# Kernel optimization log

Measured on AMD Instinct MI355X. Metric: run time of the kernel, lower is better.

The kernel has to match this reference:

```python
import jax, jax.numpy as jnp
import numpy as np

NA = 50000
NB = 50000
E = 800000
D = 256


def setup_inputs() -> dict:
    key = jax.random.key(0)
    ks = jax.random.split(key, 7)
    feature_a = jax.random.normal(ks[0], (NA, D), dtype=jnp.float32)
    feature_b = jax.random.normal(ks[1], (NB, D), dtype=jnp.float32)
    # Linear(b_dim, b_dim): store weight pre-transposed so new_emb = feature_b @ W + b
    W = jax.random.normal(ks[2], (D, D), dtype=jnp.float32) * (1.0 / np.sqrt(D))
    b = jnp.zeros((D,), dtype=jnp.float32)
    # kaiming-normal-ish init for attention vector a: [a_dim + b_dim, 1]
    a = jax.random.normal(ks[3], (2 * D, 1), dtype=jnp.float32) * np.sqrt(2.0 / (2 * D))
    edge_src = jnp.sort(jax.random.randint(ks[4], (E,), 0, NA, dtype=jnp.int32)).astype(jnp.int64)
    edge_dst = jax.random.randint(ks[5], (E,), 0, NB, dtype=jnp.int64)
    return {
        "feature_a": feature_a,
        "feature_b": feature_b,
        "W": W,
        "b": b,
        "a": a,
        "edge_src": edge_src,
        "edge_dst": edge_dst,
        "node_num_a": NA,
        "node_num_b": NB,
    }


def reference(feature_a, feature_b, W, b, a, edge_src, edge_dst, node_num_a, node_num_b):
    # new_emb = out_mlp_layer(feature_b)
    new_emb = feature_b @ W + b  # [Nb, D]

    # cat([feature_a[src], new_emb[dst]]) @ a  ==  (feature_a @ a_top)[src] + (new_emb @ a_bot)[dst]
    a_dim = feature_a.shape[1]
    a_top = a[:a_dim, 0]   # [a_dim]
    a_bot = a[a_dim:, 0]   # [b_dim]
    s_a = feature_a @ a_top   # [Na]
    s_b = new_emb @ a_bot     # [Nb]
    logits = s_a[edge_src] + s_b[edge_dst]  # [E]

    # exp(elu(x, alpha=0.1))
    elu = jnp.where(logits > 0, logits, 0.1 * jnp.expm1(logits))
    score = jnp.exp(elu)  # [E]

    # sparse mm: weighted aggregation of new_emb over edges, grouped by src
    msg = score[:, None] * new_emb[edge_dst]  # [E, D]
    agg = jax.ops.segment_sum(msg, edge_src, num_segments=node_num_a)       # [Na, D]
    row_sum = jax.ops.segment_sum(score, edge_src, num_segments=node_num_a)  # [Na]
    row_sum = jnp.where(row_sum == 0, 1.0, row_sum)[:, None]
    return agg / row_sum
```

## Files before the change

kernel.cpp:

```cpp
#include <hip/hip_runtime.h>
#include <cstdint>

#define NA_N 50000
#define NB_N 50000
#define NE_N 800000
#define DD 256

using bf8   = __attribute__((ext_vector_type(8))) short;
using f32x4 = __attribute__((ext_vector_type(4))) float;
using u16x8 = __attribute__((ext_vector_type(8))) ushort;

__device__ __forceinline__ ushort f2bf(float f) {
    uint u = __float_as_uint(f);
    uint r = (u + 0x7fffu + ((u >> 16) & 1u)) >> 16;
    return (ushort)r;
}
__device__ __forceinline__ float bf2f(ushort u) {
    return __uint_as_float(((uint)u) << 16);
}

__global__ __launch_bounds__(256) void prep_k(const float* __restrict__ W,
    ushort* __restrict__ Wt, const int* __restrict__ esrc,
    int* __restrict__ row_start)
{
    if (blockIdx.x < 16) {
        __shared__ float T[64][65];
        const int bi = blockIdx.x & 3;
        const int bj = blockIdx.x >> 2;
        const int lane = threadIdx.x & 63, w = threadIdx.x >> 6;
        for (int i = w; i < 64; i += 4)
            T[i][lane] = W[(size_t)(bi * 64 + i) * DD + bj * 64 + lane];
        __syncthreads();
        for (int i = w; i < 64; i += 4)
            Wt[(size_t)(bj * 64 + i) * DD + bi * 64 + lane] = f2bf(T[lane][i]);
    } else {
        int e = (blockIdx.x - 16) * 256 + threadIdx.x;
        if (e >= NE_N) return;
        int s    = esrc[e];
        int prev = (e == 0) ? -1 : esrc[e - 1];
        for (int r = prev + 1; r <= s; r++) row_start[r] = e;
        if (e == NE_N - 1)
            for (int r = s + 1; r <= NA_N; r++) row_start[r] = NE_N;
    }
}

__global__ __launch_bounds__(256) void gemm_mfma(
    const float* __restrict__ A, const ushort* __restrict__ Wt,
    const float* __restrict__ bias, const float* __restrict__ a_bot,
    ushort* __restrict__ C, float* __restrict__ s_b)
{
    __shared__ ushort As[64 * 264];
    __shared__ float  sdot[4][64];
    const int t  = threadIdx.x;
    const int r0 = blockIdx.x * 64;

#pragma unroll
    for (int i = 0; i < 16; i++) {
        int flat = i * 256 + t;
        int row  = flat >> 6;
        int c4   = flat & 63;
        int gr   = r0 + row; if (gr >= NB_N) gr = 0;
        float4 v = ((const float4*)(A + (size_t)gr * DD))[c4];
        ushort4 b;
        b.x = f2bf(v.x); b.y = f2bf(v.y); b.z = f2bf(v.z); b.w = f2bf(v.w);
        *(ushort4*)&As[row * 264 + c4 * 4] = b;
    }
    __syncthreads();

    const int lane = t & 63;
    const int wv   = t >> 6;
    const int lr   = lane & 15;
    const int lk   = (lane >> 4) * 8;

    f32x4 acc[4][4];
#pragma unroll
    for (int m = 0; m < 4; m++)
#pragma unroll
        for (int n = 0; n < 4; n++) acc[m][n] = (f32x4){0.f, 0.f, 0.f, 0.f};

#pragma unroll
    for (int ks = 0; ks < 8; ks++) {
        const int k0 = ks * 32;
        bf8 af[4], bb[4];
#pragma unroll
        for (int m = 0; m < 4; m++)
            af[m] = *(const bf8*)&As[(m * 16 + lr) * 264 + k0 + lk];
#pragma unroll
        for (int n = 0; n < 4; n++) {
            int col = wv * 64 + n * 16 + lr;
            bb[n] = *(const bf8*)&Wt[(size_t)col * DD + k0 + lk];
        }
#pragma unroll
        for (int m = 0; m < 4; m++)
#pragma unroll
            for (int n = 0; n < 4; n++)
                acc[m][n] = __builtin_amdgcn_mfma_f32_16x16x32_bf16(
                    af[m], bb[n], acc[m][n], 0, 0, 0);
    }

    float abv[4];
#pragma unroll
    for (int n = 0; n < 4; n++) abv[n] = a_bot[wv * 64 + n * 16 + lr];

    float part[4][4];
#pragma unroll
    for (int m = 0; m < 4; m++)
#pragma unroll
        for (int r = 0; r < 4; r++) part[m][r] = 0.f;

#pragma unroll
    for (int m = 0; m < 4; m++)
#pragma unroll
        for (int n = 0; n < 4; n++) {
            int   col = wv * 64 + n * 16 + lr;
            float bv  = bias[col];
#pragma unroll
            for (int r = 0; r < 4; r++) {
                int   rowg = r0 + m * 16 + (lane >> 4) * 4 + r;
                float v    = acc[m][n][r] + bv;
                if (rowg < NB_N) C[(size_t)rowg * DD + col] = f2bf(v);
                part[m][r] = fmaf(v, abv[n], part[m][r]);
            }
        }

#pragma unroll
    for (int m = 0; m < 4; m++)
#pragma unroll
        for (int r = 0; r < 4; r++) {
#pragma unroll
            for (int off = 1; off < 16; off <<= 1)
                part[m][r] += __shfl_xor(part[m][r], off, 64);
        }
    if (lr == 0) {
#pragma unroll
        for (int m = 0; m < 4; m++)
#pragma unroll
            for (int r = 0; r < 4; r++)
                sdot[wv][m * 16 + (lane >> 4) * 4 + r] = part[m][r];
    }
    __syncthreads();
    if (t < 64) {
        int rowg = r0 + t;
        if (rowg < NB_N)
            s_b[rowg] = sdot[0][t] + sdot[1][t] + sdot[2][t] + sdot[3][t];
    }
}

__global__ __launch_bounds__(256) void edge_agg6(
    const int* __restrict__ edst, const int* __restrict__ row_start,
    const float* __restrict__ fa, const float* __restrict__ a_top,
    const float* __restrict__ sb, const ushort* __restrict__ emb,
    float* __restrict__ out)
{
    const int lane = threadIdx.x & 63;
    const int a    = blockIdx.x * 4 + (threadIdx.x >> 6);
    if (a >= NA_N) return;

    float4 av = ((const float4*)(fa + (size_t)a * DD))[lane];
    float4 tv = ((const float4*)a_top)[lane];
    float  sa_a = av.x * tv.x + av.y * tv.y + av.z * tv.z + av.w * tv.w;
#pragma unroll
    for (int off = 1; off < 64; off <<= 1) sa_a += __shfl_xor(sa_a, off, 64);

    const int g = lane >> 4;
    const int c = lane & 15;
    const int beg = row_start[a], end = row_start[a + 1];

    float accA[8], accB[8];
#pragma unroll
    for (int j = 0; j < 8; j++) { accA[j] = 0.f; accB[j] = 0.f; }
    float rs = 0.f;

    if (beg < end) {
        const int last = end - 1;

        int   pc  = beg + g;
        int   pn  = pc + 4;
        int   dc  = edst[min(pc, last)];
        int   dn  = edst[min(pn, last)];
        float sbc = sb[dc];
        float sbn = sb[dn];
        const ushort* rc = emb + (size_t)dc * DD + c * 16;
        u16x8 ua = *(const u16x8*)rc;
        u16x8 ub = *(const u16x8*)(rc + 8);

#pragma unroll 2
        for (int e = beg; e < end; e += 4) {
            const ushort* rn = emb + (size_t)dn * DD + c * 16;
            u16x8 na = *(const u16x8*)rn;
            u16x8 nb = *(const u16x8*)(rn + 8);
            int   p2  = pn + 4;
            int   d2  = edst[min(p2, last)];
            float sb2 = sb[d2];

            float lg = sa_a + sbc;
            float el = lg > 0.f ? lg : 0.1f * (__expf(lg) - 1.f);
            float s  = (pc < end) ? __expf(el) : 0.f;

#pragma unroll
            for (int j = 0; j < 8; j++) {
                accA[j] = fmaf(s, bf2f(ua[j]), accA[j]);
                accB[j] = fmaf(s, bf2f(ub[j]), accB[j]);
            }
            rs += s;

            pc = pn;  dc = dn;  sbc = sbn;
            ua = na;  ub = nb;
            pn = p2;  dn = d2;  sbn = sb2;
        }
    }

#pragma unroll
    for (int j = 0; j < 8; j++) {
        accA[j] += __shfl_xor(accA[j], 16, 64);
        accA[j] += __shfl_xor(accA[j], 32, 64);
        accB[j] += __shfl_xor(accB[j], 16, 64);
        accB[j] += __shfl_xor(accB[j], 32, 64);
    }
    rs += __shfl_xor(rs, 16, 64);
    rs += __shfl_xor(rs, 32, 64);

    if (g == 0) {
        const float inv = (rs == 0.f) ? 1.f : (1.f / rs);
        float* op = out + (size_t)a * DD + c * 16;
        float4 o0 = { accA[0] * inv, accA[1] * inv, accA[2] * inv, accA[3] * inv };
        float4 o1 = { accA[4] * inv, accA[5] * inv, accA[6] * inv, accA[7] * inv };
        float4 o2 = { accB[0] * inv, accB[1] * inv, accB[2] * inv, accB[3] * inv };
        float4 o3 = { accB[4] * inv, accB[5] * inv, accB[6] * inv, accB[7] * inv };
        *(float4*)(op + 0)  = o0;
        *(float4*)(op + 4)  = o1;
        *(float4*)(op + 8)  = o2;
        *(float4*)(op + 12) = o3;
    }
}

extern "C" void kernel_launch(void* const* d_in, const int* in_sizes, int n_in,
                              void* d_out, int out_size, void* d_ws, size_t ws_size,
                              hipStream_t stream)
{
    const float* fa   = (const float*)d_in[0];
    const float* fb   = (const float*)d_in[1];
    const float* W    = (const float*)d_in[2];
    const float* bias = (const float*)d_in[3];
    const float* avec = (const float*)d_in[4];
    const int*   esrc = (const int*)d_in[5];
    const int*   edst = (const int*)d_in[6];
    float*       out  = (float*)d_out;

    char*   ws        = (char*)d_ws;
    ushort* emb_b     = (ushort*)ws;
    float*  s_b       = (float*)(ws + (size_t)NB_N * DD * 2);
    int*    row_start = (int*)(s_b + NB_N);
    ushort* Wt        = (ushort*)(row_start + NA_N + 2);

    prep_k   <<<16 + (NE_N + 255) / 256, 256, 0, stream>>>(W, Wt, esrc, row_start);
    gemm_mfma<<<(NB_N + 63) / 64, 256, 0, stream>>>(fb, Wt, bias, avec + DD,
                                                    emb_b, s_b);
    edge_agg6<<<(NA_N + 3) / 4, 256, 0, stream>>>(edst, row_start, fa, avec,
                                                  s_b, emb_b, out);
}
```

Baseline: 108.5 us.

## Recast edge aggregation as MFMA with one-hot score matrix and async LDS staging

Replaces the per-row wave aggregation with a block that handles 16 source rows at once. Each chunk of 32 edges forms a sparse 16x32 score matrix (bf16 one-hot by source), and the gathered destination embeddings are multiplied by it with MFMA. The embeddings are staged into double-buffered LDS through global_load_lds and read back with transposed ds_read, and the row sums come from an extra MFMA against a ones vector. This trades scalar FMAs for matrix ops and overlaps gathers with compute, but it rounds scores to bf16 and adds block-wide barriers per chunk.

```diff
diff --git a/kernel.cpp b/kernel.cpp
--- a/kernel.cpp
+++ b/kernel.cpp
@@ -8,15 +8,12 @@
 
 using bf8   = __attribute__((ext_vector_type(8))) short;
 using f32x4 = __attribute__((ext_vector_type(4))) float;
-using u16x8 = __attribute__((ext_vector_type(8))) ushort;
+using u32x2 = __attribute__((ext_vector_type(2))) unsigned int;
 
 __device__ __forceinline__ ushort f2bf(float f) {
     uint u = __float_as_uint(f);
     uint r = (u + 0x7fffu + ((u >> 16) & 1u)) >> 16;
     return (ushort)r;
-}
-__device__ __forceinline__ float bf2f(ushort u) {
-    return __uint_as_float(((uint)u) << 16);
 }
 
 __global__ __launch_bounds__(256) void prep_k(const float* __restrict__ W,
@@ -146,92 +143,155 @@
     }
 }
 
-__global__ __launch_bounds__(256) void edge_agg6(
-    const int* __restrict__ edst, const int* __restrict__ row_start,
+__global__ __launch_bounds__(256) void edge_mfma(
+    const int* __restrict__ esrc, const int* __restrict__ edst,
+    const int* __restrict__ row_start,
     const float* __restrict__ fa, const float* __restrict__ a_top,
     const float* __restrict__ sb, const ushort* __restrict__ emb,
     float* __restrict__ out)
 {
-    const int lane = threadIdx.x & 63;
-    const int a    = blockIdx.x * 4 + (threadIdx.x >> 6);
-    if (a >= NA_N) return;
-
-    float4 av = ((const float4*)(fa + (size_t)a * DD))[lane];
-    float4 tv = ((const float4*)a_top)[lane];
-    float  sa_a = av.x * tv.x + av.y * tv.y + av.z * tv.z + av.w * tv.w;
-#pragma unroll
-    for (int off = 1; off < 64; off <<= 1) sa_a += __shfl_xor(sa_a, off, 64);
-
-    const int g = lane >> 4;
-    const int c = lane & 15;
-    const int beg = row_start[a], end = row_start[a + 1];
-
-    float accA[8], accB[8];
-#pragma unroll
-    for (int j = 0; j < 8; j++) { accA[j] = 0.f; accB[j] = 0.f; }
-    float rs = 0.f;
-
-    if (beg < end) {
-        const int last = end - 1;
-
-        int   pc  = beg + g;
-        int   pn  = pc + 4;
-        int   dc  = edst[min(pc, last)];
-        int   dn  = edst[min(pn, last)];
-        float sbc = sb[dc];
-        float sbn = sb[dn];
-        const ushort* rc = emb + (size_t)dc * DD + c * 16;
-        u16x8 ua = *(const u16x8*)rc;
-        u16x8 ub = *(const u16x8*)(rc + 8);
-
-#pragma unroll 2
-        for (int e = beg; e < end; e += 4) {
-            const ushort* rn = emb + (size_t)dn * DD + c * 16;
-            u16x8 na = *(const u16x8*)rn;
-            u16x8 nb = *(const u16x8*)(rn + 8);
-            int   p2  = pn + 4;
-            int   d2  = edst[min(p2, last)];
-            float sb2 = sb[d2];
-
-            float lg = sa_a + sbc;
-            float el = lg > 0.f ? lg : 0.1f * (__expf(lg) - 1.f);
-            float s  = (pc < end) ? __expf(el) : 0.f;
-
+    __shared__ ushort Bt[2][8192];
+    __shared__ float  sa_sh[16];
+    const int t = threadIdx.x, lane = t & 63, wv = t >> 6;
+    const int a0 = blockIdx.x * 16;
+
+    {
+        int r  = t >> 4;
+        int cs = (t & 15) * 16;
+        const float4* fr = (const float4*)(fa + (size_t)(a0 + r) * DD + cs);
+        const float4* tv = (const float4*)(a_top + cs);
+        float p = 0.f;
+#pragma unroll
+        for (int j = 0; j < 4; j++) {
+            float4 x = fr[j], y = tv[j];
+            p += x.x * y.x + x.y * y.y + x.z * y.z + x.w * y.w;
+        }
+        p += __shfl_xor(p, 1, 64); p += __shfl_xor(p, 2, 64);
+        p += __shfl_xor(p, 4, 64); p += __shfl_xor(p, 8, 64);
+        if ((t & 15) == 0) sa_sh[r] = p;
+    }
+    __syncthreads();
+    const float sa_lane = sa_sh[lane & 15];
+
+    const int beg  = row_start[a0], end = row_start[a0 + 16];
+    const int nch  = (end - beg + 31) >> 5;
+    const int el   = lane & 31;
+    const int last = end - 1;
+
+    f32x4 acc0 = {0,0,0,0}, acc1 = {0,0,0,0}, acc2 = {0,0,0,0},
+          acc3 = {0,0,0,0}, racc = {0,0,0,0};
+
+    const uint b0  = (uint)(uintptr_t)&Bt[0][0];
+    const uint trb = b0 + (uint)((lane >> 4) * 4096 + wv * 512 + (lane & 15) * 8);
+
+    bf8 onesb;
+    {
+        short o = (lane & 15) == 0 ? (short)0x3F80 : (short)0;
+#pragma unroll
+        for (int j = 0; j < 8; j++) onesb[j] = o;
+    }
+
+#define STAGE(BQ, DREG)                                                        \
+    {                                                                          \
+        _Pragma("unroll")                                                      \
+        for (int i_ = 0; i_ < 4; i_++) {                                       \
+            int W_  = wv * 4 + i_;                                             \
+            int k_  = ((W_ >> 1) << 2) | ((lane >> 1) & 3);                    \
+            int dk_ = __shfl((DREG), k_, 64);                                  \
+            const ushort* gs_ = emb + (size_t)dk_ * DD                         \
+                + (W_ & 1) * 128 + ((lane >> 3) & 7) * 16 + (lane & 1) * 8;    \
+            __builtin_amdgcn_global_load_lds(                                  \
+                (const __attribute__((address_space(1))) void*)(uintptr_t)gs_, \
+                (__attribute__((address_space(3))) void*)(uint)((BQ) + (uint)(W_ * 1024)), \
+                16, 0, 0);                                                     \
+        }                                                                      \
+    }
+
+    if (nch > 0) {
+        int   i0   = min(beg + el, last);
+        int   sr_c = esrc[i0] - a0;
+        int   d0   = edst[i0];
+        int   i1   = min(beg + 32 + el, last);
+        int   d_n  = edst[i1];
+        int   sr_n = esrc[i1] - a0;
+        float sb_c = sb[d0];
+        STAGE(b0, d0);
+
+        for (int tc = 0; tc < nch; ++tc) {
+            const int p = tc & 1;
+
+            bool  val = (beg + tc * 32 + el) < end;
+            float lg  = __shfl(sa_lane, sr_c, 64) + sb_c;
+            float elu = lg > 0.f ? lg : 0.1f * (__expf(lg) - 1.f);
+            float s   = val ? __expf(elu) : 0.f;
+            uint pack = (uint)f2bf(s) | ((uint)sr_c << 16);
+            bf8 af;
 #pragma unroll
             for (int j = 0; j < 8; j++) {
-                accA[j] = fmaf(s, bf2f(ua[j]), accA[j]);
-                accB[j] = fmaf(s, bf2f(ub[j]), accB[j]);
+                uint v = (uint)__shfl((int)pack, ((lane >> 4) << 3) + j, 64);
+                af[j]  = (short)(((v >> 16) == (uint)(lane & 15))
+                                     ? (ushort)(v & 0xFFFFu) : (ushort)0);
             }
-            rs += s;
-
-            pc = pn;  dc = dn;  sbc = sbn;
-            ua = na;  ub = nb;
-            pn = p2;  dn = d2;  sbn = sb2;
-        }
-    }
-
-#pragma unroll
-    for (int j = 0; j < 8; j++) {
-        accA[j] += __shfl_xor(accA[j], 16, 64);
-        accA[j] += __shfl_xor(accA[j], 32, 64);
-        accB[j] += __shfl_xor(accB[j], 16, 64);
-        accB[j] += __shfl_xor(accB[j], 32, 64);
-    }
-    rs += __shfl_xor(rs, 16, 64);
-    rs += __shfl_xor(rs, 32, 64);
-
-    if (g == 0) {
-        const float inv = (rs == 0.f) ? 1.f : (1.f / rs);
-        float* op = out + (size_t)a * DD + c * 16;
-        float4 o0 = { accA[0] * inv, accA[1] * inv, accA[2] * inv, accA[3] * inv };
-        float4 o1 = { accA[4] * inv, accA[5] * inv, accA[6] * inv, accA[7] * inv };
-        float4 o2 = { accB[0] * inv, accB[1] * inv, accB[2] * inv, accB[3] * inv };
-        float4 o3 = { accB[4] * inv, accB[5] * inv, accB[6] * inv, accB[7] * inv };
-        *(float4*)(op + 0)  = o0;
-        *(float4*)(op + 4)  = o1;
-        *(float4*)(op + 8)  = o2;
-        *(float4*)(op + 12) = o3;
-    }
+
+            const bool more = (tc + 1) < nch;
+            int d_nn = 0, sr_nn = 0; float sb_nn = 0.f;
+            if (more) {
+                sb_nn   = sb[d_n];
+                int i2  = min(beg + (tc + 2) * 32 + el, last);
+                d_nn    = edst[i2];
+                sr_nn   = esrc[i2] - a0;
+                uint bq = b0 + (uint)((p ^ 1) * 16384);
+                STAGE(bq, d_n);
+                asm volatile("s_waitcnt vmcnt(7)" ::: "memory");
+            } else {
+                asm volatile("s_waitcnt vmcnt(0)" ::: "memory");
+            }
+            __builtin_amdgcn_s_barrier();
+
+            const uint base = trb + (uint)(p * 16384);
+            u32x2 t0, t1, t2, t3, t4, t5, t6, t7;
+            asm volatile("ds_read_b64_tr_b16 %0, %1" : "=v"(t0) : "v"(base));
+            asm volatile("ds_read_b64_tr_b16 %0, %1" : "=v"(t1) : "v"(base + 2048u));
+            asm volatile("ds_read_b64_tr_b16 %0, %1" : "=v"(t2) : "v"(base + 128u));
+            asm volatile("ds_read_b64_tr_b16 %0, %1" : "=v"(t3) : "v"(base + 2176u));
+            asm volatile("ds_read_b64_tr_b16 %0, %1" : "=v"(t4) : "v"(base + 256u));
+            asm volatile("ds_read_b64_tr_b16 %0, %1" : "=v"(t5) : "v"(base + 2304u));
+            asm volatile("ds_read_b64_tr_b16 %0, %1" : "=v"(t6) : "v"(base + 384u));
+            asm volatile("ds_read_b64_tr_b16 %0, %1" : "=v"(t7) : "v"(base + 2432u));
+            asm volatile("s_waitcnt lgkmcnt(0)" ::: "memory");
+            __builtin_amdgcn_sched_barrier(0);
+
+            union { bf8 v; u32x2 h[2]; } U;
+            bf8 bf0, bf1, bf2, bf3;
+            U.h[0] = t0; U.h[1] = t1; bf0 = U.v;
+            U.h[0] = t2; U.h[1] = t3; bf1 = U.v;
+            U.h[0] = t4; U.h[1] = t5; bf2 = U.v;
+            U.h[0] = t6; U.h[1] = t7; bf3 = U.v;
+
+            acc0 = __builtin_amdgcn_mfma_f32_16x16x32_bf16(af, bf0, acc0, 0, 0, 0);
+            acc1 = __builtin_amdgcn_mfma_f32_16x16x32_bf16(af, bf1, acc1, 0, 0, 0);
+            acc2 = __builtin_amdgcn_mfma_f32_16x16x32_bf16(af, bf2, acc2, 0, 0, 0);
+            acc3 = __builtin_amdgcn_mfma_f32_16x16x32_bf16(af, bf3, acc3, 0, 0, 0);
+            racc = __builtin_amdgcn_mfma_f32_16x16x32_bf16(af, onesb, racc, 0, 0, 0);
+
+            __builtin_amdgcn_s_barrier();
+
+            sr_c = sr_n; sb_c = sb_nn; d_n = d_nn; sr_n = sr_nn;
+        }
+    }
+
+#pragma unroll
+    for (int reg = 0; reg < 4; reg++) {
+        float rsv = __shfl(racc[reg], lane & 48, 64);
+        float iv  = (rsv == 0.f) ? 0.f : (1.f / rsv);
+        int   row = a0 + (lane >> 4) * 4 + reg;
+        float* op = out + (size_t)row * DD + wv * 64 + (lane & 15);
+        op[0]  = acc0[reg] * iv;
+        op[16] = acc1[reg] * iv;
+        op[32] = acc2[reg] * iv;
+        op[48] = acc3[reg] * iv;
+    }
+#undef STAGE
 }
 
 extern "C" void kernel_launch(void* const* d_in, const int* in_sizes, int n_in,
@@ -256,6 +316,6 @@
     prep_k   <<<16 + (NE_N + 255) / 256, 256, 0, stream>>>(W, Wt, esrc, row_start);
     gemm_mfma<<<(NB_N + 63) / 64, 256, 0, stream>>>(fb, Wt, bias, avec + DD,
                                                     emb_b, s_b);
-    edge_agg6<<<(NA_N + 3) / 4, 256, 0, stream>>>(edst, row_start, fa, avec,
-                                                  s_b, emb_b, out);
-}
+    edge_mfma<<<NA_N / 16, 256, 0, stream>>>(esrc, edst, row_start, fa, avec,
+                                             s_b, emb_b, out);
+}
```

New measurement: 113.6 us. 1.05x slower.

## Move row_start build into GEMM launch and use nontemporal loads/stores

Applied to the files above, without the earlier changes.

Moves the CSR row_start construction out of the W-transpose prep kernel into extra blocks of the GEMM launch, so the prep kernel is tiny and the edge scan runs alongside the GEMM. It also marks streaming reads of feature_b, feature_a and edge_dst, and the output writes, as nontemporal to reduce cache pollution. The GEMM kernel now carries extra blocks with an early-exit path, which could change scheduling. Nontemporal hints may help or hurt the cache behaviour of the gather-heavy aggregation kernel.

```diff
diff --git a/kernel.cpp b/kernel.cpp
--- a/kernel.cpp
+++ b/kernel.cpp
@@ -5,6 +5,7 @@
 #define NB_N 50000
 #define NE_N 800000
 #define DD 256
+#define GEMM_NBLK 782
 
 using bf8   = __attribute__((ext_vector_type(8))) short;
 using f32x4 = __attribute__((ext_vector_type(4))) float;
@@ -20,37 +21,39 @@
 }
 
 __global__ __launch_bounds__(256) void prep_k(const float* __restrict__ W,
-    ushort* __restrict__ Wt, const int* __restrict__ esrc,
-    int* __restrict__ row_start)
-{
-    if (blockIdx.x < 16) {
-        __shared__ float T[64][65];
-        const int bi = blockIdx.x & 3;
-        const int bj = blockIdx.x >> 2;
-        const int lane = threadIdx.x & 63, w = threadIdx.x >> 6;
-        for (int i = w; i < 64; i += 4)
-            T[i][lane] = W[(size_t)(bi * 64 + i) * DD + bj * 64 + lane];
-        __syncthreads();
-        for (int i = w; i < 64; i += 4)
-            Wt[(size_t)(bj * 64 + i) * DD + bi * 64 + lane] = f2bf(T[lane][i]);
-    } else {
-        int e = (blockIdx.x - 16) * 256 + threadIdx.x;
+                                              ushort* __restrict__ Wt)
+{
+    __shared__ float T[64][65];
+    const int bi = blockIdx.x & 3;
+    const int bj = blockIdx.x >> 2;
+    const int lane = threadIdx.x & 63, w = threadIdx.x >> 6;
+    for (int i = w; i < 64; i += 4)
+        T[i][lane] = W[(size_t)(bi * 64 + i) * DD + bj * 64 + lane];
+    __syncthreads();
+    for (int i = w; i < 64; i += 4)
+        Wt[(size_t)(bj * 64 + i) * DD + bi * 64 + lane] = f2bf(T[lane][i]);
+}
+
+__global__ __launch_bounds__(256) void gemm_mfma(
+    const float* __restrict__ A, const ushort* __restrict__ Wt,
+    const float* __restrict__ bias, const float* __restrict__ a_bot,
+    ushort* __restrict__ C, float* __restrict__ s_b,
+    const int* __restrict__ esrc, int* __restrict__ row_start)
+{
+    __shared__ ushort As[64 * 264];
+    __shared__ float  sdot[4][64];
+
+    if (blockIdx.x >= GEMM_NBLK) {
+        int e = (blockIdx.x - GEMM_NBLK) * 256 + threadIdx.x;
         if (e >= NE_N) return;
         int s    = esrc[e];
         int prev = (e == 0) ? -1 : esrc[e - 1];
         for (int r = prev + 1; r <= s; r++) row_start[r] = e;
         if (e == NE_N - 1)
             for (int r = s + 1; r <= NA_N; r++) row_start[r] = NE_N;
-    }
-}
-
-__global__ __launch_bounds__(256) void gemm_mfma(
-    const float* __restrict__ A, const ushort* __restrict__ Wt,
-    const float* __restrict__ bias, const float* __restrict__ a_bot,
-    ushort* __restrict__ C, float* __restrict__ s_b)
-{
-    __shared__ ushort As[64 * 264];
-    __shared__ float  sdot[4][64];
+        return;
+    }
+
     const int t  = threadIdx.x;
     const int r0 = blockIdx.x * 64;
 
@@ -60,9 +63,10 @@
         int row  = flat >> 6;
         int c4   = flat & 63;
         int gr   = r0 + row; if (gr >= NB_N) gr = 0;
-        float4 v = ((const float4*)(A + (size_t)gr * DD))[c4];
+        f32x4 v = __builtin_nontemporal_load(
+                      ((const f32x4*)(A + (size_t)gr * DD)) + c4);
         ushort4 b;
-        b.x = f2bf(v.x); b.y = f2bf(v.y); b.z = f2bf(v.z); b.w = f2bf(v.w);
+        b.x = f2bf(v[0]); b.y = f2bf(v[1]); b.z = f2bf(v[2]); b.w = f2bf(v[3]);
         *(ushort4*)&As[row * 264 + c4 * 4] = b;
     }
     __syncthreads();
@@ -146,7 +150,7 @@
     }
 }
 
-__global__ __launch_bounds__(256) void edge_agg6(
+__global__ __launch_bounds__(256) void edge_agg7(
     const int* __restrict__ edst, const int* __restrict__ row_start,
     const float* __restrict__ fa, const float* __restrict__ a_top,
     const float* __restrict__ sb, const ushort* __restrict__ emb,
@@ -156,9 +160,9 @@
     const int a    = blockIdx.x * 4 + (threadIdx.x >> 6);
     if (a >= NA_N) return;
 
-    float4 av = ((const float4*)(fa + (size_t)a * DD))[lane];
-    float4 tv = ((const float4*)a_top)[lane];
-    float  sa_a = av.x * tv.x + av.y * tv.y + av.z * tv.z + av.w * tv.w;
+    f32x4 av = __builtin_nontemporal_load(((const f32x4*)(fa + (size_t)a * DD)) + lane);
+    f32x4 tv = *(((const f32x4*)a_top) + lane);
+    float sa_a = av[0] * tv[0] + av[1] * tv[1] + av[2] * tv[2] + av[3] * tv[3];
 #pragma unroll
     for (int off = 1; off < 64; off <<= 1) sa_a += __shfl_xor(sa_a, off, 64);
 
@@ -176,8 +180,8 @@
 
         int   pc  = beg + g;
         int   pn  = pc + 4;
-        int   dc  = edst[min(pc, last)];
-        int   dn  = edst[min(pn, last)];
+        int   dc  = __builtin_nontemporal_load(edst + min(pc, last));
+        int   dn  = __builtin_nontemporal_load(edst + min(pn, last));
         float sbc = sb[dc];
         float sbn = sb[dn];
         const ushort* rc = emb + (size_t)dc * DD + c * 16;
@@ -190,7 +194,7 @@
             u16x8 na = *(const u16x8*)rn;
             u16x8 nb = *(const u16x8*)(rn + 8);
             int   p2  = pn + 4;
-            int   d2  = edst[min(p2, last)];
+            int   d2  = __builtin_nontemporal_load(edst + min(p2, last));
             float sb2 = sb[d2];
 
             float lg = sa_a + sbc;
@@ -223,14 +227,14 @@
     if (g == 0) {
         const float inv = (rs == 0.f) ? 1.f : (1.f / rs);
         float* op = out + (size_t)a * DD + c * 16;
-        float4 o0 = { accA[0] * inv, accA[1] * inv, accA[2] * inv, accA[3] * inv };
-        float4 o1 = { accA[4] * inv, accA[5] * inv, accA[6] * inv, accA[7] * inv };
-        float4 o2 = { accB[0] * inv, accB[1] * inv, accB[2] * inv, accB[3] * inv };
-        float4 o3 = { accB[4] * inv, accB[5] * inv, accB[6] * inv, accB[7] * inv };
-        *(float4*)(op + 0)  = o0;
-        *(float4*)(op + 4)  = o1;
-        *(float4*)(op + 8)  = o2;
-        *(float4*)(op + 12) = o3;
+        f32x4 o0 = { accA[0] * inv, accA[1] * inv, accA[2] * inv, accA[3] * inv };
+        f32x4 o1 = { accA[4] * inv, accA[5] * inv, accA[6] * inv, accA[7] * inv };
+        f32x4 o2 = { accB[0] * inv, accB[1] * inv, accB[2] * inv, accB[3] * inv };
+        f32x4 o3 = { accB[4] * inv, accB[5] * inv, accB[6] * inv, accB[7] * inv };
+        __builtin_nontemporal_store(o0, (f32x4*)(op + 0));
+        __builtin_nontemporal_store(o1, (f32x4*)(op + 4));
+        __builtin_nontemporal_store(o2, (f32x4*)(op + 8));
+        __builtin_nontemporal_store(o3, (f32x4*)(op + 12));
     }
 }
 
@@ -253,9 +257,9 @@
     int*    row_start = (int*)(s_b + NB_N);
     ushort* Wt        = (ushort*)(row_start + NA_N + 2);
 
-    prep_k   <<<16 + (NE_N + 255) / 256, 256, 0, stream>>>(W, Wt, esrc, row_start);
-    gemm_mfma<<<(NB_N + 63) / 64, 256, 0, stream>>>(fb, Wt, bias, avec + DD,
-                                                    emb_b, s_b);
-    edge_agg6<<<(NA_N + 3) / 4, 256, 0, stream>>>(edst, row_start, fa, avec,
+    prep_k   <<<16, 256, 0, stream>>>(W, Wt);
+    gemm_mfma<<<GEMM_NBLK + (NE_N + 255) / 256, 256, 0, stream>>>(
+        fb, Wt, bias, avec + DD, emb_b, s_b, esrc, row_start);
+    edge_agg7<<<(NA_N + 3) / 4, 256, 0, stream>>>(edst, row_start, fa, avec,
                                                   s_b, emb_b, out);
 }
```

Result: slower. 111.8 us (+3.1%).
